# Kernel optimization log

Measured on AMD Instinct MI355X. Metric: run time of the kernel, lower is better.

## Reference

```python
import jax, jax.numpy as jnp
import numpy as np
import math

DIM = 1024
B, S = 4, 2048

def setup_inputs() -> dict:
    key = jax.random.key(0)
    ks = jax.random.split(key, 4)
    scale = 1.0 / math.sqrt(DIM)
    X = jax.random.normal(ks[0], (B, S, DIM), dtype=jnp.float32)
    W_in = jax.random.normal(ks[1], (3 * DIM, DIM), dtype=jnp.float32) * scale
    b_in = jnp.zeros((3 * DIM,), dtype=jnp.float32)
    W_out = jax.random.normal(ks[2], (DIM, DIM), dtype=jnp.float32) * scale
    b_out = jnp.zeros((DIM,), dtype=jnp.float32)
    attention_mask = jnp.ones((B, 1, S), dtype=jnp.int32)
    return {"X": X, "attention_mask": attention_mask, "W_in": W_in,
            "b_in": b_in, "W_out": W_out, "b_out": b_out}

def reference(X, attention_mask, W_in, b_in, W_out, b_out):
    # in_proj: [B,S,3*DIM]
    qkv = jnp.einsum('bsd,ed->bse', X, W_in) + b_in
    Q, K, V = jnp.split(qkv, 3, axis=-1)
    # scores: [B,S,S]
    scores = jnp.einsum('bqd,bkd->bqk', Q, K)
    # masked_fill happens BEFORE the /sqrt(dim) scaling in the original
    scores = jnp.where(attention_mask == 0, jnp.float32(-1e20), scores)
    attn = jax.nn.softmax(scores / jnp.float32(math.sqrt(DIM)), axis=-1)
    # Dropout(0.1) treated as identity (eval-mode reference)
    out = jnp.einsum('bqk,bkd->bqd', attn, V)
    return jnp.einsum('bsd,od->bso', out, W_out) + b_out
```

## Files before the change

kernel.cpp:

```cpp
#include <hip/hip_runtime.h>
#include <stdint.h>

#define AS1 __attribute__((address_space(1)))
#define AS3 __attribute__((address_space(3)))

typedef __bf16 bf16x8 __attribute__((ext_vector_type(8)));
typedef float f32x16 __attribute__((ext_vector_type(16)));

__device__ __forceinline__ unsigned short f2bf(float f) {
  unsigned u = __float_as_uint(f);
  u += 0x7FFF + ((u >> 16) & 1);
  return (unsigned short)(u >> 16);
}
__device__ __forceinline__ float bf2f(unsigned short h) {
  return __uint_as_float(((unsigned)h) << 16);
}

__global__ __launch_bounds__(256) void cast_kernel(const float* __restrict__ in,
                                                   unsigned short* __restrict__ out,
                                                   int n4) {
  int i = blockIdx.x * 256 + threadIdx.x;
  if (i >= n4) return;
  float4 v = reinterpret_cast<const float4*>(in)[i];
  ushort4 o;
  o.x = f2bf(v.x); o.y = f2bf(v.y); o.z = f2bf(v.z); o.w = f2bf(v.w);
  reinterpret_cast<ushort4*>(out)[i] = o;
}

template<int OUT_BF16>
__global__ __launch_bounds__(256, 2) void gemm_bt(
    const unsigned short* __restrict__ A, long lda, long strideA,
    const unsigned short* __restrict__ B, long ldb, long strideB,
    void* __restrict__ Cv, long ldc, long strideC,
    const float* __restrict__ bias, int K) {
  __shared__ unsigned short sA[128 * 64];
  __shared__ unsigned short sB[128 * 64];
  const int t = threadIdx.x;
  const int lane = t & 63;
  const int wave = t >> 6;

  const unsigned short* Ab = A + (size_t)blockIdx.z * strideA + (size_t)blockIdx.y * 128 * lda;
  const unsigned short* Bb = B + (size_t)blockIdx.z * strideB + (size_t)blockIdx.x * 128 * ldb;

  const int srow = t >> 3;
  const int schunk = (t & 7) ^ (srow & 7);
  const unsigned short* aptr = Ab + (size_t)srow * lda + schunk * 8;
  const unsigned short* bptr = Bb + (size_t)srow * ldb + schunk * 8;
  char* ldsA0 = (char*)&sA[0] + wave * 1024;
  char* ldsB0 = (char*)&sB[0] + wave * 1024;

  f32x16 acc[2][2];
#pragma unroll
  for (int i = 0; i < 2; i++)
#pragma unroll
    for (int j = 0; j < 2; j++)
#pragma unroll
      for (int r = 0; r < 16; r++) acc[i][j][r] = 0.f;

  const int wm = (wave >> 1) * 64;
  const int wn = (wave & 1) * 64;
  const int r31 = lane & 31;
  const int half = lane >> 5;
  const int swz = r31 & 7;

  int offA[2][4], offB[2][4];
#pragma unroll
  for (int i = 0; i < 2; i++)
#pragma unroll
    for (int s = 0; s < 4; s++) {
      offA[i][s] = (wm + i * 32 + r31) * 128 + (((2 * s + half) ^ swz) * 16);
      offB[i][s] = (wn + i * 32 + r31) * 128 + (((2 * s + half) ^ swz) * 16);
    }

  for (int k0 = 0; k0 < K; k0 += 64) {
    __syncthreads();
#pragma unroll
    for (int o = 0; o < 4; o++) {
      __builtin_amdgcn_global_load_lds((AS1 void*)(aptr + (size_t)o * 32 * lda + k0),
                                       (AS3 void*)(ldsA0 + o * 4096), 16, 0, 0);
      __builtin_amdgcn_global_load_lds((AS1 void*)(bptr + (size_t)o * 32 * ldb + k0),
                                       (AS3 void*)(ldsB0 + o * 4096), 16, 0, 0);
    }
    __syncthreads();
#pragma unroll
    for (int s = 0; s < 4; s++) {
      bf16x8 af[2], bfv[2];
#pragma unroll
      for (int i = 0; i < 2; i++) {
        af[i]  = *reinterpret_cast<const bf16x8*>((const char*)sA + offA[i][s]);
        bfv[i] = *reinterpret_cast<const bf16x8*>((const char*)sB + offB[i][s]);
      }
#pragma unroll
      for (int i = 0; i < 2; i++)
#pragma unroll
        for (int j = 0; j < 2; j++)
          acc[i][j] = __builtin_amdgcn_mfma_f32_32x32x16_bf16(af[i], bfv[j], acc[i][j], 0, 0, 0);
    }
  }

#pragma unroll
  for (int i = 0; i < 2; i++) {
    int gmb = blockIdx.y * 128 + wm + i * 32;
#pragma unroll
    for (int j = 0; j < 2; j++) {
      int gn = blockIdx.x * 128 + wn + j * 32 + r31;
      float bv = bias ? bias[gn] : 0.0f;
#pragma unroll
      for (int r = 0; r < 16; r++) {
        int row = (r & 3) + 8 * (r >> 2) + 4 * half;
        float val = acc[i][j][r] + bv;
        size_t off = (size_t)blockIdx.z * strideC + (size_t)(gmb + row) * ldc + gn;
        if (OUT_BF16)
          ((unsigned short*)Cv)[off] = f2bf(val);
        else
          ((float*)Cv)[off] = val;
      }
    }
  }
}

__global__ __launch_bounds__(256) void transpose_v(const unsigned short* __restrict__ qkv,
                                                   unsigned short* __restrict__ vt) {
  __shared__ unsigned short tile[64][68];
  int t = threadIdx.x;
  int s0 = blockIdx.x * 64, d0 = blockIdx.y * 64, b = blockIdx.z;
  const unsigned short* V = qkv + (size_t)b * 2048 * 3072 + 2048;
  unsigned short* Vt = vt + (size_t)b * 1024 * 2048;
  int r = t >> 4, c = (t & 15) * 4;
#pragma unroll
  for (int i = 0; i < 4; i++) {
    int s = r + i * 16;
    ushort4 v4 = *reinterpret_cast<const ushort4*>(&V[(size_t)(s0 + s) * 3072 + d0 + c]);
    tile[s][c] = v4.x; tile[s][c + 1] = v4.y; tile[s][c + 2] = v4.z; tile[s][c + 3] = v4.w;
  }
  __syncthreads();
#pragma unroll
  for (int i = 0; i < 4; i++) {
    int d = r + i * 16;
    ushort4 o;
    o.x = tile[c][d]; o.y = tile[c + 1][d]; o.z = tile[c + 2][d]; o.w = tile[c + 3][d];
    *reinterpret_cast<ushort4*>(&Vt[(size_t)(d0 + d) * 2048 + s0 + c]) = o;
  }
}

__global__ __launch_bounds__(256) void softmax_kernel(unsigned short* __restrict__ P,
                                                      const int* __restrict__ mask) {
  __shared__ float red[8];
  const int S = 2048;
  int row = blockIdx.x;
  int b = row >> 11;
  unsigned short* prow = P + (size_t)row * S;
  const int* mrow = mask + (size_t)b * S;
  int t = threadIdx.x;
  int base = t * 8;
  uint4 raw = *reinterpret_cast<const uint4*>(&prow[base]);
  int4 m0 = *reinterpret_cast<const int4*>(&mrow[base]);
  int4 m1 = *reinterpret_cast<const int4*>(&mrow[base + 4]);
  unsigned short us[8];
  us[0] = raw.x & 0xffff; us[1] = raw.x >> 16;
  us[2] = raw.y & 0xffff; us[3] = raw.y >> 16;
  us[4] = raw.z & 0xffff; us[5] = raw.z >> 16;
  us[6] = raw.w & 0xffff; us[7] = raw.w >> 16;
  int mk[8] = {m0.x, m0.y, m0.z, m0.w, m1.x, m1.y, m1.z, m1.w};
  float l[8];
  float mx = -3.4e38f;
#pragma unroll
  for (int j = 0; j < 8; j++) {
    float v = bf2f(us[j]);
    v = (mk[j] == 0) ? -1e20f : v;
    l[j] = v * 0.03125f;
    mx = fmaxf(mx, l[j]);
  }
#pragma unroll
  for (int o = 32; o >= 1; o >>= 1) mx = fmaxf(mx, __shfl_xor(mx, o, 64));
  if ((t & 63) == 0) red[t >> 6] = mx;
  __syncthreads();
  mx = fmaxf(fmaxf(red[0], red[1]), fmaxf(red[2], red[3]));
  float e[8], s = 0.f;
#pragma unroll
  for (int j = 0; j < 8; j++) { e[j] = __expf(l[j] - mx); s += e[j]; }
#pragma unroll
  for (int o = 32; o >= 1; o >>= 1) s += __shfl_xor(s, o, 64);
  if ((t & 63) == 0) red[4 + (t >> 6)] = s;
  __syncthreads();
  s = red[4] + red[5] + red[6] + red[7];
  float inv = 1.0f / s;
  unsigned short eo[8];
#pragma unroll
  for (int j = 0; j < 8; j++) eo[j] = f2bf(e[j] * inv);
  uint4 outv;
  outv.x = eo[0] | ((unsigned)eo[1] << 16);
  outv.y = eo[2] | ((unsigned)eo[3] << 16);
  outv.z = eo[4] | ((unsigned)eo[5] << 16);
  outv.w = eo[6] | ((unsigned)eo[7] << 16);
  *reinterpret_cast<uint4*>(&prow[base]) = outv;
}

extern "C" void kernel_launch(void* const* d_in, const int* in_sizes, int n_in,
                              void* d_out, int out_size, void* d_ws, size_t ws_size,
                              hipStream_t stream) {
  const float* X = (const float*)d_in[0];
  const int* mask = (const int*)d_in[1];
  const float* W_in = (const float*)d_in[2];
  const float* b_in = (const float*)d_in[3];
  const float* W_out = (const float*)d_in[4];
  const float* b_out = (const float*)d_in[5];
  float* out = (float*)d_out;

  const int S = 2048, D = 1024;
  char* w = (char*)d_ws;
  unsigned short* Xb  = (unsigned short*)w;
  unsigned short* Wib = (unsigned short*)(w + 16777216);
  unsigned short* Wob = (unsigned short*)(w + 16777216 + 6291456);
  unsigned short* QKV = (unsigned short*)(w + 16777216 + 6291456 + 2097152);
  unsigned short* P   = (unsigned short*)(w + 16777216 + 6291456 + 2097152 + 50331648);
  unsigned short* Vt  = (unsigned short*)(w + 16777216 + 6291456 + 2097152 + 50331648 + 33554432);
  unsigned short* Ob  = Xb;

  cast_kernel<<<8192, 256, 0, stream>>>(X, Xb, 2097152);
  cast_kernel<<<3072, 256, 0, stream>>>(W_in, Wib, 786432);
  cast_kernel<<<1024, 256, 0, stream>>>(W_out, Wob, 262144);

  gemm_bt<1><<<dim3(24, 64, 1), 256, 0, stream>>>(Xb, D, 0, Wib, D, 0,
                                                  QKV, 3 * D, 0, b_in, D);
  transpose_v<<<dim3(32, 16, 4), 256, 0, stream>>>(QKV, Vt);
  gemm_bt<1><<<dim3(16, 16, 4), 256, 0, stream>>>(QKV, 3 * D, (long)S * 3 * D,
                                                  QKV + D, 3 * D, (long)S * 3 * D,
                                                  P, S, (long)S * S, nullptr, D);
  softmax_kernel<<<8192, 256, 0, stream>>>(P, mask);
  gemm_bt<1><<<dim3(8, 16, 4), 256, 0, stream>>>(P, S, (long)S * S,
                                                 Vt, S, (long)D * S,
                                                 Ob, D, (long)S * D, nullptr, S);
  gemm_bt<0><<<dim3(8, 64, 1), 256, 0, stream>>>(Ob, D, 0, Wob, D, 0,
                                                 out, D, 0, b_out, D);
}
```

Before: 302.1 us.

## Double-buffer GEMM LDS tiles with register-staged global prefetch

Replaces direct global-to-LDS async loads with register-staged loads into two LDS buffers, so the tile for step k+2 is fetched from global memory and the tile for step k+1 is written to LDS while MFMA runs on step k. This removes one of the two barriers per K step and hides global load latency behind compute. In exchange it doubles LDS use to 64KB per block, which may limit occupancy below the launch-bounds target of two blocks, and adds VGPR pressure from the staging registers.

```diff
diff --git a/kernel.cpp b/kernel.cpp
--- a/kernel.cpp
+++ b/kernel.cpp
@@ -1,8 +1,5 @@
 #include <hip/hip_runtime.h>
 #include <stdint.h>
-
-#define AS1 __attribute__((address_space(1)))
-#define AS3 __attribute__((address_space(3)))
 
 typedef __bf16 bf16x8 __attribute__((ext_vector_type(8)));
 typedef float f32x16 __attribute__((ext_vector_type(16)));
@@ -33,8 +30,8 @@
     const unsigned short* __restrict__ B, long ldb, long strideB,
     void* __restrict__ Cv, long ldc, long strideC,
     const float* __restrict__ bias, int K) {
-  __shared__ unsigned short sA[128 * 64];
-  __shared__ unsigned short sB[128 * 64];
+  __shared__ unsigned short sA[2][128 * 64];
+  __shared__ unsigned short sB[2][128 * 64];
   const int t = threadIdx.x;
   const int lane = t & 63;
   const int wave = t >> 6;
@@ -42,12 +39,42 @@
   const unsigned short* Ab = A + (size_t)blockIdx.z * strideA + (size_t)blockIdx.y * 128 * lda;
   const unsigned short* Bb = B + (size_t)blockIdx.z * strideB + (size_t)blockIdx.x * 128 * ldb;
 
-  const int srow = t >> 3;
-  const int schunk = (t & 7) ^ (srow & 7);
-  const unsigned short* aptr = Ab + (size_t)srow * lda + schunk * 8;
-  const unsigned short* bptr = Bb + (size_t)srow * ldb + schunk * 8;
-  char* ldsA0 = (char*)&sA[0] + wave * 1024;
-  char* ldsB0 = (char*)&sB[0] + wave * 1024;
+  const int r0 = t >> 2;
+  const int q = t & 3;
+  const unsigned short* aptr = Ab + (size_t)r0 * lda + q * 8;
+  const unsigned short* bptr = Bb + (size_t)r0 * ldb + q * 8;
+  const int sw = r0 & 7;
+  int woff[4];
+  woff[0] = r0 * 128 + ((q ^ sw) * 16);
+  woff[1] = r0 * 128 + (((q + 4) ^ sw) * 16);
+  woff[2] = (r0 + 64) * 128 + ((q ^ sw) * 16);
+  woff[3] = (r0 + 64) * 128 + (((q + 4) ^ sw) * 16);
+
+  uint4 ra[4], rb[4];
+#define LOAD_TILE(k0)                                                              \
+  {                                                                                \
+    ra[0] = *reinterpret_cast<const uint4*>(aptr + (k0));                          \
+    ra[1] = *reinterpret_cast<const uint4*>(aptr + (k0) + 32);                     \
+    ra[2] = *reinterpret_cast<const uint4*>(aptr + 64 * lda + (k0));               \
+    ra[3] = *reinterpret_cast<const uint4*>(aptr + 64 * lda + (k0) + 32);          \
+    rb[0] = *reinterpret_cast<const uint4*>(bptr + (k0));                          \
+    rb[1] = *reinterpret_cast<const uint4*>(bptr + (k0) + 32);                     \
+    rb[2] = *reinterpret_cast<const uint4*>(bptr + 64 * ldb + (k0));               \
+    rb[3] = *reinterpret_cast<const uint4*>(bptr + 64 * ldb + (k0) + 32);          \
+  }
+#define STORE_TILE(buf)                                                            \
+  {                                                                                \
+    char* ba = (char*)&sA[buf][0];                                                 \
+    char* bb = (char*)&sB[buf][0];                                                 \
+    *reinterpret_cast<uint4*>(ba + woff[0]) = ra[0];                               \
+    *reinterpret_cast<uint4*>(ba + woff[1]) = ra[1];                               \
+    *reinterpret_cast<uint4*>(ba + woff[2]) = ra[2];                               \
+    *reinterpret_cast<uint4*>(ba + woff[3]) = ra[3];                               \
+    *reinterpret_cast<uint4*>(bb + woff[0]) = rb[0];                               \
+    *reinterpret_cast<uint4*>(bb + woff[1]) = rb[1];                               \
+    *reinterpret_cast<uint4*>(bb + woff[2]) = rb[2];                               \
+    *reinterpret_cast<uint4*>(bb + woff[3]) = rb[3];                               \
+  }
 
   f32x16 acc[2][2];
 #pragma unroll
@@ -72,23 +99,25 @@
       offB[i][s] = (wn + i * 32 + r31) * 128 + (((2 * s + half) ^ swz) * 16);
     }
 
-  for (int k0 = 0; k0 < K; k0 += 64) {
-    __syncthreads();
-#pragma unroll
-    for (int o = 0; o < 4; o++) {
-      __builtin_amdgcn_global_load_lds((AS1 void*)(aptr + (size_t)o * 32 * lda + k0),
-                                       (AS3 void*)(ldsA0 + o * 4096), 16, 0, 0);
-      __builtin_amdgcn_global_load_lds((AS1 void*)(bptr + (size_t)o * 32 * ldb + k0),
-                                       (AS3 void*)(ldsB0 + o * 4096), 16, 0, 0);
-    }
-    __syncthreads();
+  const int niter = K >> 6;
+  LOAD_TILE(0);
+  STORE_TILE(0);
+  LOAD_TILE(64);
+  __syncthreads();
+
+  for (int k = 0; k < niter; k++) {
+    const int cur = k & 1;
+    if (k + 1 < niter) STORE_TILE(cur ^ 1);
+    if (k + 2 < niter) LOAD_TILE((k + 2) << 6);
+    const char* cA = (const char*)&sA[cur][0];
+    const char* cB = (const char*)&sB[cur][0];
 #pragma unroll
     for (int s = 0; s < 4; s++) {
       bf16x8 af[2], bfv[2];
 #pragma unroll
       for (int i = 0; i < 2; i++) {
-        af[i]  = *reinterpret_cast<const bf16x8*>((const char*)sA + offA[i][s]);
-        bfv[i] = *reinterpret_cast<const bf16x8*>((const char*)sB + offB[i][s]);
+        af[i]  = *reinterpret_cast<const bf16x8*>(cA + offA[i][s]);
+        bfv[i] = *reinterpret_cast<const bf16x8*>(cB + offB[i][s]);
       }
 #pragma unroll
       for (int i = 0; i < 2; i++)
@@ -96,6 +125,7 @@
         for (int j = 0; j < 2; j++)
           acc[i][j] = __builtin_amdgcn_mfma_f32_32x32x16_bf16(af[i], bfv[j], acc[i][j], 0, 0, 0);
     }
+    __syncthreads();
   }
 
 #pragma unroll
@@ -117,6 +147,8 @@
       }
     }
   }
+#undef LOAD_TILE
+#undef STORE_TILE
 }
 
 __global__ __launch_bounds__(256) void transpose_v(const unsigned short* __restrict__ qkv,
```

After: 559.4 us. 85.1% more time.
